# Optimization experiments

Measured on AMD Instinct MI355X. Metric: run time of the kernel, lower is better.

Reference implementation:

```python
import jax, jax.numpy as jnp
import numpy as np

D_MODEL = 1024
NUM_HEADS = 16
HEAD_DIM = D_MODEL // NUM_HEADS
SCALING = HEAD_DIM ** -0.5


def setup_inputs() -> dict:
    key = jax.random.key(0)
    ks = jax.random.split(key, 13)
    B, L = 4, 1024
    d = D_MODEL
    inp = {
        'query': jax.random.normal(ks[0], (B, L, d), jnp.float32),
        'key': jax.random.normal(ks[1], (B, L, d), jnp.float32),
        'value': jax.random.normal(ks[2], (B, L, d), jnp.float32),
        'key_padding_mask': jax.random.randint(ks[3], (B, L), 0, 2).astype(bool),
        # Linear params, torch convention W: [out, in]
        'Wq': jax.random.normal(ks[4], (d, d), jnp.float32) * (d ** -0.5),
        'bq': jax.random.normal(ks[5], (d,), jnp.float32) * 0.01,
        'Wk': jax.random.normal(ks[6], (d, d), jnp.float32) * (d ** -0.5),
        'bk': jax.random.normal(ks[7], (d,), jnp.float32) * 0.01,
        'Wv': jax.random.normal(ks[8], (d, d), jnp.float32) * (d ** -0.5),
        'bv': jax.random.normal(ks[9], (d,), jnp.float32) * 0.01,
        'Wo': jax.random.normal(ks[10], (d, d), jnp.float32) * (d ** -0.5),
        'bo': jax.random.normal(ks[11], (d,), jnp.float32) * 0.01,
    }
    return inp


def _split_heads(x, B, L):
    # [B, L, d_model] -> [B, H, L, head_dim]
    return x.reshape(B, L, NUM_HEADS, HEAD_DIM).transpose(0, 2, 1, 3)


def reference(query, key, value, key_padding_mask, Wq, bq, Wk, bk, Wv, bv, Wo, bo):
    B, Lq, _ = query.shape
    Lk = key.shape[1]
    Q = (query @ Wq.T + bq) * SCALING
    K = key @ Wk.T + bk
    V = value @ Wv.T + bv
    Q = _split_heads(Q, B, Lq)
    K = _split_heads(K, B, Lk)
    V = _split_heads(V, B, Lk)
    scores = jnp.einsum('bhqd,bhkd->bhqk', Q, K)
    scores = jnp.where(key_padding_mask[:, None, None, :], -jnp.inf, scores)
    w = jax.nn.softmax(scores, axis=-1)  # masked positions -> exactly 0
    # counterfactual_type == 'uniform': replace each nonzero weight by the row
    # mean over nonzero entries (sum / count), keep zeros as-is.
    nz = w != 0
    cnt = jnp.maximum(nz.sum(axis=-1, keepdims=True), 1).astype(w.dtype)
    uni = w.sum(axis=-1, keepdims=True) / cnt
    attn_weights = jnp.where(nz, uni, w)
    ctx = jnp.einsum('bhqk,bhkd->bhqd', attn_weights, V)
    ctx = ctx.transpose(0, 2, 1, 3).reshape(B, Lq, D_MODEL)
    output = ctx @ Wo.T + bo
    return output, attn_weights
```

## Files before the change

### kernel.cpp

```cpp
#include <hip/hip_runtime.h>


#define BATCH 4
#define LSEQ  1024
#define DMOD  1024
#define NHEAD 16
#define HQ    (NHEAD * LSEQ)

__global__ void k_cnt(const int* __restrict__ mask, int* __restrict__ cnt) {
    int b = blockIdx.x;
    int local = 0;
    for (int k = threadIdx.x; k < LSEQ; k += 256)
        local += (mask[b * LSEQ + k] == 0);
    __shared__ int sh[256];
    sh[threadIdx.x] = local;
    __syncthreads();
    for (int s = 128; s > 0; s >>= 1) {
        if (threadIdx.x < s) sh[threadIdx.x] += sh[threadIdx.x + s];
        __syncthreads();
    }
    if (threadIdx.x == 0) cnt[b] = max(sh[0], 1);
}

__global__ void k_vsum(const float* __restrict__ value,
                       const int* __restrict__ mask,
                       float* __restrict__ vsum) {
    int b = blockIdx.y;
    int d = threadIdx.x;
    int k0 = blockIdx.x * 16;
    float acc = 0.f;
    for (int kk = 0; kk < 16; ++kk) {
        int k = k0 + kk;
        if (mask[b * LSEQ + k] == 0)
            acc += value[((size_t)b * LSEQ + k) * DMOD + d];
    }
    atomicAdd(&vsum[b * DMOD + d], acc);
}

__global__ void k_matvec(const float* __restrict__ x,
                         const float* __restrict__ W,
                         const float* __restrict__ bias,
                         const int* __restrict__ cnt,
                         int useInvCnt,
                         float* __restrict__ y) {
    int b = blockIdx.y;
    int wave = threadIdx.x >> 6;
    int lane = threadIdx.x & 63;
    int o = blockIdx.x * 4 + wave;
    float scale = useInvCnt ? (1.0f / (float)cnt[b]) : 1.0f;
    const float4* x4 = (const float4*)(x + (size_t)b * DMOD);
    const float4* w4 = (const float4*)(W + (size_t)o * DMOD);
    float acc = 0.f;
    for (int i = lane; i < DMOD / 4; i += 64) {
        float4 a = x4[i];
        float4 w = w4[i];
        acc += a.x * w.x + a.y * w.y + a.z * w.z + a.w * w.w;
    }
    for (int off = 32; off > 0; off >>= 1)
        acc += __shfl_down(acc, off, 64);
    if (lane == 0) y[(size_t)b * DMOD + o] = acc * scale + bias[o];
}

__global__ void k_out(const float* __restrict__ outrow, float* __restrict__ out) {
    int b = blockIdx.y;
    int t = threadIdx.x;
    float4 v = ((const float4*)(outrow + (size_t)b * DMOD))[t];
    float4* base = (float4*)out + ((size_t)b * LSEQ + (size_t)blockIdx.x * 16) * (DMOD / 4) + t;
    #pragma unroll
    for (int r = 0; r < 16; ++r)
        base[(size_t)r * (DMOD / 4)] = v;
}

__global__ void k_attn(const int* __restrict__ mask,
                       const int* __restrict__ cnt,
                       float* __restrict__ attn) {
    int b = blockIdx.y;
    int t = threadIdx.x;
    float inv = 1.0f / (float)cnt[b];
    const int* mrow = mask + (size_t)b * LSEQ;
    float4 pat;
    pat.x = mrow[t * 4 + 0] ? 0.f : inv;
    pat.y = mrow[t * 4 + 1] ? 0.f : inv;
    pat.z = mrow[t * 4 + 2] ? 0.f : inv;
    pat.w = mrow[t * 4 + 3] ? 0.f : inv;
    float4* base = (float4*)attn +
        ((size_t)b * HQ + (size_t)blockIdx.x * 64) * (DMOD / 4) + t;
    #pragma unroll
    for (int r = 0; r < 64; ++r)
        base[(size_t)r * (DMOD / 4)] = pat;
}

extern "C" void kernel_launch(void* const* d_in, const int* in_sizes, int n_in,
                              void* d_out, int out_size, void* d_ws, size_t ws_size,
                              hipStream_t stream) {
    const float* value = (const float*)d_in[2];
    const int*   mask  = (const int*)d_in[3];
    const float* Wv    = (const float*)d_in[8];
    const float* bv    = (const float*)d_in[9];
    const float* Wo    = (const float*)d_in[10];
    const float* bo    = (const float*)d_in[11];

    float* out  = (float*)d_out;
    float* attn = out + (size_t)BATCH * LSEQ * DMOD;

    float* wsf    = (float*)d_ws;
    int*   cnt    = (int*)wsf;
    float* vsum   = wsf + 16;
    float* ctx    = vsum + BATCH * DMOD;
    float* outrow = ctx + BATCH * DMOD;

    hipMemsetAsync(d_ws, 0, (16 + BATCH * DMOD) * sizeof(float), stream);

    k_cnt   <<<BATCH, 256, 0, stream>>>(mask, cnt);
    k_vsum  <<<dim3(64, BATCH), 1024, 0, stream>>>(value, mask, vsum);
    k_matvec<<<dim3(DMOD / 4, BATCH), 256, 0, stream>>>(vsum, Wv, bv, cnt, 1, ctx);
    k_matvec<<<dim3(DMOD / 4, BATCH), 256, 0, stream>>>(ctx, Wo, bo, cnt, 0, outrow);
    k_out   <<<dim3(LSEQ / 16, BATCH), 256, 0, stream>>>(outrow, out);
    k_attn  <<<dim3(HQ / 64, BATCH), 256, 0, stream>>>(mask, cnt, attn);
}
```

Before: 353.6 us.

## Fuse mask count into vsum, merge output writers, use nontemporal stores

The mask-count kernel is folded into the value-sum kernel, which now loads float4 per thread with 256 threads and atomically adds its per-block count. The matvec maps one output row per block across all four batches, so each W row is shared by the four batch waves. The two broadcast-write kernels (output rows and attention pattern) are merged into one launch that writes through nontemporal stores, aiming to cut launch overhead and cache pollution on the large attention write. The trade-off is more atomics, and the fused writer handles both the attention and output writes in one launch.

```diff
diff --git a/kernel.cpp b/kernel.cpp
--- a/kernel.cpp
+++ b/kernel.cpp
@@ -5,36 +5,37 @@
 #define LSEQ  1024
 #define DMOD  1024
 #define NHEAD 16
-#define HQ    (NHEAD * LSEQ)
+#define ROWS_PER_B (NHEAD * LSEQ)
+#define D4    (DMOD / 4)
 
-__global__ void k_cnt(const int* __restrict__ mask, int* __restrict__ cnt) {
-    int b = blockIdx.x;
-    int local = 0;
-    for (int k = threadIdx.x; k < LSEQ; k += 256)
-        local += (mask[b * LSEQ + k] == 0);
-    __shared__ int sh[256];
-    sh[threadIdx.x] = local;
-    __syncthreads();
-    for (int s = 128; s > 0; s >>= 1) {
-        if (threadIdx.x < s) sh[threadIdx.x] += sh[threadIdx.x + s];
-        __syncthreads();
-    }
-    if (threadIdx.x == 0) cnt[b] = max(sh[0], 1);
-}
+typedef float f32x4 __attribute__((ext_vector_type(4)));
 
 __global__ void k_vsum(const float* __restrict__ value,
                        const int* __restrict__ mask,
-                       float* __restrict__ vsum) {
+                       float* __restrict__ vsum,
+                       int* __restrict__ cnt) {
     int b = blockIdx.y;
-    int d = threadIdx.x;
+    int t = threadIdx.x;
     int k0 = blockIdx.x * 16;
-    float acc = 0.f;
+    const int* mrow = mask + (size_t)b * LSEQ;
+    f32x4 acc = {0.f, 0.f, 0.f, 0.f};
+    int c = 0;
+    #pragma unroll
     for (int kk = 0; kk < 16; ++kk) {
         int k = k0 + kk;
-        if (mask[b * LSEQ + k] == 0)
-            acc += value[((size_t)b * LSEQ + k) * DMOD + d];
+        if (mrow[k] == 0) {
+            const f32x4* row = (const f32x4*)(value + ((size_t)b * LSEQ + k) * DMOD);
+            f32x4 v = row[t];
+            acc += v;
+            ++c;
+        }
     }
-    atomicAdd(&vsum[b * DMOD + d], acc);
+    float* dst = vsum + (size_t)b * DMOD + t * 4;
+    atomicAdd(dst + 0, acc.x);
+    atomicAdd(dst + 1, acc.y);
+    atomicAdd(dst + 2, acc.z);
+    atomicAdd(dst + 3, acc.w);
+    if (t == 0) atomicAdd(&cnt[b], c);
 }
 
 __global__ void k_matvec(const float* __restrict__ x,
@@ -43,51 +44,57 @@
                          const int* __restrict__ cnt,
                          int useInvCnt,
                          float* __restrict__ y) {
-    int b = blockIdx.y;
-    int wave = threadIdx.x >> 6;
+    int o = blockIdx.x;
+    int b = threadIdx.x >> 6;
     int lane = threadIdx.x & 63;
-    int o = blockIdx.x * 4 + wave;
-    float scale = useInvCnt ? (1.0f / (float)cnt[b]) : 1.0f;
-    const float4* x4 = (const float4*)(x + (size_t)b * DMOD);
-    const float4* w4 = (const float4*)(W + (size_t)o * DMOD);
+    const f32x4* x4 = (const f32x4*)(x + (size_t)b * DMOD);
+    const f32x4* w4 = (const f32x4*)(W + (size_t)o * DMOD);
     float acc = 0.f;
-    for (int i = lane; i < DMOD / 4; i += 64) {
-        float4 a = x4[i];
-        float4 w = w4[i];
+    #pragma unroll
+    for (int i = lane; i < D4; i += 64) {
+        f32x4 a = x4[i];
+        f32x4 w = w4[i];
         acc += a.x * w.x + a.y * w.y + a.z * w.z + a.w * w.w;
     }
+    #pragma unroll
     for (int off = 32; off > 0; off >>= 1)
         acc += __shfl_down(acc, off, 64);
-    if (lane == 0) y[(size_t)b * DMOD + o] = acc * scale + bias[o];
+    if (lane == 0) {
+        float scale = useInvCnt ? (1.0f / (float)max(cnt[b], 1)) : 1.0f;
+        y[(size_t)b * DMOD + o] = acc * scale + bias[o];
+    }
 }
 
-__global__ void k_out(const float* __restrict__ outrow, float* __restrict__ out) {
+__global__ void k_write(const int* __restrict__ mask,
+                        const int* __restrict__ cnt,
+                        const float* __restrict__ outrow,
+                        float* __restrict__ out,
+                        float* __restrict__ attn) {
     int b = blockIdx.y;
     int t = threadIdx.x;
-    float4 v = ((const float4*)(outrow + (size_t)b * DMOD))[t];
-    float4* base = (float4*)out + ((size_t)b * LSEQ + (size_t)blockIdx.x * 16) * (DMOD / 4) + t;
-    #pragma unroll
-    for (int r = 0; r < 16; ++r)
-        base[(size_t)r * (DMOD / 4)] = v;
-}
-
-__global__ void k_attn(const int* __restrict__ mask,
-                       const int* __restrict__ cnt,
-                       float* __restrict__ attn) {
-    int b = blockIdx.y;
-    int t = threadIdx.x;
-    float inv = 1.0f / (float)cnt[b];
-    const int* mrow = mask + (size_t)b * LSEQ;
-    float4 pat;
-    pat.x = mrow[t * 4 + 0] ? 0.f : inv;
-    pat.y = mrow[t * 4 + 1] ? 0.f : inv;
-    pat.z = mrow[t * 4 + 2] ? 0.f : inv;
-    pat.w = mrow[t * 4 + 3] ? 0.f : inv;
-    float4* base = (float4*)attn +
-        ((size_t)b * HQ + (size_t)blockIdx.x * 64) * (DMOD / 4) + t;
-    #pragma unroll
-    for (int r = 0; r < 64; ++r)
-        base[(size_t)r * (DMOD / 4)] = pat;
+    int bx = blockIdx.x;
+    if (bx < 512) {
+        float inv = 1.0f / (float)max(cnt[b], 1);
+        const int* mrow = mask + (size_t)b * LSEQ;
+        f32x4 pat;
+        pat.x = mrow[t * 4 + 0] ? 0.f : inv;
+        pat.y = mrow[t * 4 + 1] ? 0.f : inv;
+        pat.z = mrow[t * 4 + 2] ? 0.f : inv;
+        pat.w = mrow[t * 4 + 3] ? 0.f : inv;
+        f32x4* base = (f32x4*)attn +
+            ((size_t)b * ROWS_PER_B + (size_t)bx * 32) * D4 + t;
+        #pragma unroll
+        for (int r = 0; r < 32; ++r)
+            __builtin_nontemporal_store(pat, base + (size_t)r * D4);
+    } else {
+        int obx = bx - 512;
+        f32x4 v = ((const f32x4*)(outrow + (size_t)b * DMOD))[t];
+        f32x4* base = (f32x4*)out +
+            ((size_t)b * LSEQ + (size_t)obx * 32) * D4 + t;
+        #pragma unroll
+        for (int r = 0; r < 32; ++r)
+            __builtin_nontemporal_store(v, base + (size_t)r * D4);
+    }
 }
 
 extern "C" void kernel_launch(void* const* d_in, const int* in_sizes, int n_in,
@@ -109,12 +116,10 @@
     float* ctx    = vsum + BATCH * DMOD;
     float* outrow = ctx + BATCH * DMOD;
 
-    hipMemsetAsync(d_ws, 0, (16 + BATCH * DMOD) * sizeof(float), stream);
+    (void)hipMemsetAsync(d_ws, 0, (16 + BATCH * DMOD) * sizeof(float), stream);
 
-    k_cnt   <<<BATCH, 256, 0, stream>>>(mask, cnt);
-    k_vsum  <<<dim3(64, BATCH), 1024, 0, stream>>>(value, mask, vsum);
-    k_matvec<<<dim3(DMOD / 4, BATCH), 256, 0, stream>>>(vsum, Wv, bv, cnt, 1, ctx);
-    k_matvec<<<dim3(DMOD / 4, BATCH), 256, 0, stream>>>(ctx, Wo, bo, cnt, 0, outrow);
-    k_out   <<<dim3(LSEQ / 16, BATCH), 256, 0, stream>>>(outrow, out);
-    k_attn  <<<dim3(HQ / 64, BATCH), 256, 0, stream>>>(mask, cnt, attn);
+    k_vsum  <<<dim3(64, BATCH), 256, 0, stream>>>(value, mask, vsum, cnt);
+    k_matvec<<<DMOD, 256, 0, stream>>>(vsum, Wv, bv, cnt, 1, ctx);
+    k_matvec<<<DMOD, 256, 0, stream>>>(ctx, Wo, bo, cnt, 0, outrow);
+    k_write <<<dim3(512 + 32, BATCH), 256, 0, stream>>>(mask, cnt, outrow, out, attn);
 }
```

Measured after the change: 350.6 us. About the same (-0.8%).
